# Kernel optimization log

Hardware: AMD Instinct MI355X
Metric: run time of the kernel (lower is better)

The kernel has to match this reference:

```python
import jax, jax.numpy as jnp
import numpy as np


def diff_x(inp, r):
    left = inp[:, :, r:2 * r + 1]
    middle = inp[:, :, 2 * r + 1:] - inp[:, :, :-2 * r - 1]
    right = inp[:, :, -1:] - inp[:, :, -2 * r - 1:-r - 1]
    return jnp.concatenate([left, middle, right], axis=2)


def diff_y(inp, r):
    left = inp[:, :, :, r:2 * r + 1]
    middle = inp[:, :, :, 2 * r + 1:] - inp[:, :, :, :-2 * r - 1]
    right = inp[:, :, :, -1:] - inp[:, :, :, -2 * r - 1:-r - 1]
    return jnp.concatenate([left, middle, right], axis=3)


def setup_inputs() -> dict:
    key = jax.random.key(0)
    B, C, H, W = 8, 3, 1080, 1920
    x = jax.random.normal(key, (B, C, H, W), dtype=jnp.float32)
    return {"x": x, "r": 4}


def reference(x, r):
    # Box filter: cumsum + sliced diff along H, then along W.
    return diff_y(jnp.cumsum(diff_x(jnp.cumsum(x, axis=2), r), axis=3), r)
```

## Files before the change

### kernel.cpp

```cpp
#include <hip/hip_runtime.h>


#define W_IMG 1920
#define H_IMG 1080
#define SH 135
#define OUTC 56
#define R 4

__global__ __launch_bounds__(256) void box9_wave(const float* __restrict__ x,
                                                 float* __restrict__ out) {
    const int lane = threadIdx.x & 63;
    const int wv   = threadIdx.x >> 6;
    const int strip = blockIdx.x * 4 + wv;
    const int outc0 = strip * OUTC;
    if (outc0 >= W_IMG) return;
    const int seg = blockIdx.y;
    const int img = blockIdx.z;
    const long base = (long)img * (H_IMG * W_IMG);

    const int  cin    = outc0 - R + lane;
    const bool colOK  = (cin >= 0) && (cin < W_IMG);
    const int  outcol = outc0 + lane;
    const bool stOK   = (lane < OUTC) && (outcol < W_IMG);

    const int row0 = seg * SH;
    const float* px = x + base + (long)(row0 - R) * W_IMG + cin;
    float*       po = out + base + (long)row0 * W_IMG + outcol;

    float ring[9];
    float vsum = 0.0f;

#pragma unroll
    for (int t = 0; t < 8; ++t) {
        int row = row0 - R + t;
        float v = 0.0f;
        if (row >= 0 && colOK) v = px[0];
        ring[t] = v;
        vsum += v;
        px += W_IMG;
    }

    for (int chunk = 0; chunk < SH; chunk += 9) {
#pragma unroll
        for (int j = 0; j < 9; ++j) {
            const int i = chunk + j;
            int row = row0 + i + R;
            float v = 0.0f;
            if (row < H_IMG && colOK) v = px[0];
            px += W_IMG;
            vsum += v;
            ring[(j + 8) % 9] = v;
            float s1 = vsum + __shfl_down(vsum, 1);
            float s2 = s1 + __shfl_down(s1, 2);
            float s4 = s2 + __shfl_down(s2, 4);
            float h  = s4 + __shfl_down(vsum, 8);
            if (stOK) po[0] = h;
            po += W_IMG;
            vsum -= ring[j];
        }
    }
}

extern "C" void kernel_launch(void* const* d_in, const int* in_sizes, int n_in,
                              void* d_out, int out_size, void* d_ws, size_t ws_size,
                              hipStream_t stream) {
    const float* x = (const float*)d_in[0];
    float* out = (float*)d_out;
    dim3 grid(9, 8, 24);
    box9_wave<<<grid, 256, 0, stream>>>(x, out);
}
```

Measured before the change: 375.1 us.

## Process four columns per lane with float4 loads and stores in box filter

Each lane now loads and stores float4 vectors covering four adjacent columns, so a wave spans 240 output columns instead of 56. The horizontal 9-tap sum is rebuilt from in-register partial sums plus five shuffles. Vertical segments shrink from 135 to 27 rows to raise the block count. The intent is to cut per-element load/store instructions and the redundant halo reads, at the cost of more register pressure and more vertical halo overlap from the shorter segments.

Measured after the change: 352.9 us. 1.06x faster.

```diff
diff --git a/kernel.cpp b/kernel.cpp
--- a/kernel.cpp
+++ b/kernel.cpp
@@ -3,60 +3,74 @@
 
 #define W_IMG 1920
 #define H_IMG 1080
-#define SH 135
-#define OUTC 56
+#define SH 27
 #define R 4
 
-__global__ __launch_bounds__(256) void box9_wave(const float* __restrict__ x,
-                                                 float* __restrict__ out) {
-    const int lane = threadIdx.x & 63;
-    const int wv   = threadIdx.x >> 6;
+__global__ void box9_wave4(const float* __restrict__ x,
+                           float* __restrict__ out) {
+    const int lane  = threadIdx.x & 63;
+    const int wv    = threadIdx.x >> 6;
     const int strip = blockIdx.x * 4 + wv;
-    const int outc0 = strip * OUTC;
-    if (outc0 >= W_IMG) return;
-    const int seg = blockIdx.y;
-    const int img = blockIdx.z;
+    const int seg   = blockIdx.y;
+    const int img   = blockIdx.z;
     const long base = (long)img * (H_IMG * W_IMG);
 
-    const int  cin    = outc0 - R + lane;
-    const bool colOK  = (cin >= 0) && (cin < W_IMG);
-    const int  outcol = outc0 + lane;
-    const bool stOK   = (lane < OUTC) && (outcol < W_IMG);
+    const int  cin_raw = strip * 240 - 4 + 4 * lane;
+    const int  cin     = min(max(cin_raw, 0), W_IMG - 4);
+    const bool colOK   = (cin_raw >= 0) && (cin_raw + 3 < W_IMG);
+    const int  cout    = strip * 240 + 4 * lane;
+    const bool stOK    = (lane < 60);
 
     const int row0 = seg * SH;
-    const float* px = x + base + (long)(row0 - R) * W_IMG + cin;
-    float*       po = out + base + (long)row0 * W_IMG + outcol;
+    const float* pcol = x + base + cin;
+    float* po = out + base + (long)row0 * W_IMG + cout;
 
-    float ring[9];
-    float vsum = 0.0f;
+    float4 ring[9];
+    float4 vs = {0.f, 0.f, 0.f, 0.f};
 
 #pragma unroll
     for (int t = 0; t < 8; ++t) {
-        int row = row0 - R + t;
-        float v = 0.0f;
-        if (row >= 0 && colOK) v = px[0];
+        const int row = row0 - R + t;
+        const int rc  = max(row, 0);
+        float4 v = *(const float4*)(pcol + (long)rc * W_IMG);
+        if (row < 0 || !colOK) { v.x = 0.f; v.y = 0.f; v.z = 0.f; v.w = 0.f; }
         ring[t] = v;
-        vsum += v;
-        px += W_IMG;
+        vs.x += v.x; vs.y += v.y; vs.z += v.z; vs.w += v.w;
     }
 
     for (int chunk = 0; chunk < SH; chunk += 9) {
 #pragma unroll
         for (int j = 0; j < 9; ++j) {
-            const int i = chunk + j;
-            int row = row0 + i + R;
-            float v = 0.0f;
-            if (row < H_IMG && colOK) v = px[0];
-            px += W_IMG;
-            vsum += v;
+            const int row = row0 + chunk + j + R;
+            const int rc  = min(row, H_IMG - 1);
+            float4 v = *(const float4*)(pcol + (long)rc * W_IMG);
+            if (row >= H_IMG || !colOK) { v.x = 0.f; v.y = 0.f; v.z = 0.f; v.w = 0.f; }
+            vs.x += v.x; vs.y += v.y; vs.z += v.z; vs.w += v.w;
             ring[(j + 8) % 9] = v;
-            float s1 = vsum + __shfl_down(vsum, 1);
-            float s2 = s1 + __shfl_down(s1, 2);
-            float s4 = s2 + __shfl_down(s2, 4);
-            float h  = s4 + __shfl_down(vsum, 8);
-            if (stOK) po[0] = h;
+
+            const float s3 = vs.w;
+            const float s2 = vs.z + s3;
+            const float s1 = vs.y + s2;
+            const float S  = vs.x + s1;
+            const float p2 = vs.x + vs.y;
+            const float p3 = p2 + vs.z;
+
+            const float T  = __shfl_down(S, 1);
+            const float q1 = __shfl_down(vs.x, 2);
+            const float q2 = __shfl_down(p2, 2);
+            const float q3 = __shfl_down(p3, 2);
+            const float q4 = __shfl_down(S, 2);
+
+            float4 h;
+            h.x = S  + T + q1;
+            h.y = s1 + T + q2;
+            h.z = s2 + T + q3;
+            h.w = s3 + T + q4;
+            if (stOK) *(float4*)po = h;
             po += W_IMG;
-            vsum -= ring[j];
+
+            const float4 old = ring[j];
+            vs.x -= old.x; vs.y -= old.y; vs.z -= old.z; vs.w -= old.w;
         }
     }
 }
@@ -66,6 +80,6 @@
                               hipStream_t stream) {
     const float* x = (const float*)d_in[0];
     float* out = (float*)d_out;
-    dim3 grid(9, 8, 24);
-    box9_wave<<<grid, 256, 0, stream>>>(x, out);
+    dim3 grid(2, 40, 24);
+    box9_wave4<<<grid, 256, 0, stream>>>(x, out);
 }
```
